# Kernel tuning notes

Hardware: AMD Instinct MI355X
Metric: run time of the kernel (lower is better)

## Reference

```python
import jax, jax.numpy as jnp
import numpy as np

B, N, C = 8, 4096, 768
H, M = 12, 64          # num_heads, num_landmarks
D = C // H             # head_dim = 64


def setup_inputs() -> dict:
    key = jax.random.key(0)
    k1, k2, k3, k4 = jax.random.split(key, 4)
    s = 0.02
    return {
        "x": jax.random.normal(k1, (B, N, C), dtype=jnp.float32),
        "w_qkv": jax.random.normal(k2, (3 * C, C), dtype=jnp.float32) * s,
        "w_proj": jax.random.normal(k3, (C, C), dtype=jnp.float32) * s,
        "b_proj": jax.random.normal(k4, (C,), dtype=jnp.float32) * s,
    }


def iterative_inv(mat, n_iter=6):
    # mat: [B, H, M, M]; Newton-Schulz cubic iteration for pseudo-inverse
    I = jnp.eye(mat.shape[-1], dtype=mat.dtype)
    K = mat
    # init: K^T / max_j(sum_i K_ij)  per (B,H)
    scale = jnp.max(jnp.sum(K, axis=-2), axis=-1)[:, :, None, None]
    V = jnp.swapaxes(K, -1, -2) / scale
    for _ in range(n_iter):
        KV = K @ V
        V = 0.25 * V @ (13.0 * I - KV @ (15.0 * I - KV @ (7.0 * I - KV)))
    return V


def reference(x, w_qkv, w_proj, b_proj):
    b, n, c = x.shape
    qkv = (x @ w_qkv.T).reshape(b, n, 3, H, D).transpose(2, 0, 3, 1, 4)  # [3,B,H,N,D]
    Q, K, V = qkv[0], qkv[1], qkv[2]
    Q = Q / (D ** 0.5)
    # landmark pooling (N % M == 0 path): segment means of length N//M
    Kl = K.reshape(b, H, M, n // M, D).mean(axis=-2)  # [B,H,M,D]
    Ql = Q.reshape(b, H, M, n // M, D).mean(axis=-2)  # [B,H,M,D]
    kernel1 = jax.nn.softmax(jnp.einsum('bhnd,bhmd->bhnm', Q, Kl), axis=-1)   # [B,H,N,M]
    kernel2 = jax.nn.softmax(jnp.einsum('bhmd,bhld->bhml', Ql, Kl), axis=-1)  # [B,H,M,M]
    kernel3 = jax.nn.softmax(jnp.einsum('bhmd,bhnd->bhmn', Ql, K), axis=-1)   # [B,H,M,N]
    SV = (kernel1 @ iterative_inv(kernel2)) @ (kernel3 @ V)  # [B,H,N,D]
    SV = SV.transpose(0, 2, 1, 3).reshape(b, n, c)
    out = SV @ w_proj.T + b_proj
    out = out + V.transpose(0, 2, 1, 3).reshape(b, n, c)
    return out
```

## Files before the change

kernel.cpp:

```cpp
#include <hip/hip_runtime.h>
#include <hip/hip_bf16.h>
#include <stdint.h>

typedef __bf16 bf16;
typedef __bf16 bf16x8 __attribute__((ext_vector_type(8)));
typedef __bf16 bf16x4 __attribute__((ext_vector_type(4)));
typedef float f32x4 __attribute__((ext_vector_type(4)));

#define B_ 8
#define N_ 4096
#define C_ 768
#define H_ 12
#define M_ 64
#define D_ 64
#define NT_ 32768
#define C3_ 2304

typedef __attribute__((address_space(3))) void lds_void_t;
typedef const __attribute__((address_space(1))) void gvoid_t;

__device__ __forceinline__ void gl_lds16(const void* gsrc, void* ldst) {
  __builtin_amdgcn_global_load_lds((gvoid_t*)(uintptr_t)gsrc,
                                   (lds_void_t*)(uintptr_t)ldst, 16, 0, 0);
}

__device__ __forceinline__ f32x4 mfma16(bf16x8 a, bf16x8 b, f32x4 c) {
  return __builtin_amdgcn_mfma_f32_16x16x32_bf16(a, b, c, 0, 0, 0);
}

__global__ void k_cvt(const float* __restrict__ in, bf16* __restrict__ out, int n4) {
  const int stride = gridDim.x * blockDim.x;
  for (int i = blockIdx.x * blockDim.x + threadIdx.x; i < n4; i += stride) {
    f32x4 v = *(const f32x4*)(in + (size_t)i * 4);
    bf16x4 o;
    o[0] = (bf16)v[0]; o[1] = (bf16)v[1]; o[2] = (bf16)v[2]; o[3] = (bf16)v[3];
    *(bf16x4*)(out + (size_t)i * 4) = o;
  }
}

__global__ __launch_bounds__(512, 2) void k_qkv(
    const bf16* __restrict__ xbf, const bf16* __restrict__ wbf,
    bf16* __restrict__ Qb, bf16* __restrict__ Kb, bf16* __restrict__ Vb,
    float* __restrict__ Qlf, float* __restrict__ Klf)
{
  __shared__ bf16 As[4][8192];
  __shared__ bf16 Bs[4][8192];
  const int t = threadIdx.x;
  const int wave = t >> 6, lane = t & 63;
  const int l15 = lane & 15, l16 = lane >> 4;

  const int bid = blockIdx.x;
  const int swz = (bid & 7) * 144 + (bid >> 3);
  const int bt = swz / 9;
  const int ct = swz % 9;
  const int row0 = bt * 256, col0 = ct * 256;
  const int wr = wave >> 2, wc = wave & 3;

  const int srow = t >> 2;
  const int scol = (((t & 3) ^ ((t >> 3) & 3)) << 3);
  const bf16* gaBase = xbf + (size_t)(row0 + srow) * C_ + scol;
  const bf16* gbBase = wbf + (size_t)(col0 + srow) * C_ + scol;

  const int arow = wr * 128 + l15;
  const int aoff = arow * 32 + ((l16 ^ ((l15 >> 1) & 3)) << 3);
  const int brow = wc * 64 + l15;
  const int boff = brow * 32 + ((l16 ^ ((l15 >> 1) & 3)) << 3);

  f32x4 acc[8][4] = {};

#define BAR() { __builtin_amdgcn_sched_barrier(0); __builtin_amdgcn_s_barrier(); __builtin_amdgcn_sched_barrier(0); }
#define VMW8 asm volatile("s_waitcnt vmcnt(8)" ::: "memory")
#define VMW4 asm volatile("s_waitcnt vmcnt(4)" ::: "memory")
#define VMW0 asm volatile("s_waitcnt vmcnt(0)" ::: "memory")

#define STAGE_HALF(kt3, c) {                                                     \
    const int sb_ = (kt3) & 3;                                                   \
    gl_lds16(gaBase + (size_t)((c) * 128) * C_ + (kt3) * 32,                     \
             &As[sb_][(c) * 4096 + t * 8]);                                      \
    gl_lds16(gbBase + (size_t)((c) * 128) * C_ + (kt3) * 32,                     \
             &Bs[sb_][(c) * 4096 + t * 8]); }

#define KSTEP(kt, DO_STAGE, VMW_) {                                              \
    const bf16* as_ = As[(kt) & 3];                                              \
    const bf16* bs_ = Bs[(kt) & 3];                                              \
    if (DO_STAGE) STAGE_HALF((kt) + 3, 0);                                       \
    bf16x8 bfr[4], afr[4];                                                       \
    _Pragma("unroll")                                                            \
    for (int j = 0; j < 4; ++j) bfr[j] = *(const bf16x8*)&bs_[boff + j * 512];   \
    _Pragma("unroll")                                                            \
    for (int i = 0; i < 4; ++i) afr[i] = *(const bf16x8*)&as_[aoff + i * 512];   \
    BAR();                                                                       \
    __builtin_amdgcn_s_setprio(1);                                               \
    _Pragma("unroll")                                                            \
    for (int i = 0; i < 4; ++i)                                                  \
      _Pragma("unroll")                                                          \
      for (int j = 0; j < 4; ++j)                                                \
        acc[i][j] = mfma16(afr[i], bfr[j], acc[i][j]);                           \
    __builtin_amdgcn_s_setprio(0);                                               \
    BAR();                                                                       \
    if (DO_STAGE) STAGE_HALF((kt) + 3, 1);                                       \
    _Pragma("unroll")                                                            \
    for (int i = 0; i < 4; ++i)                                                  \
      afr[i] = *(const bf16x8*)&as_[aoff + (4 + i) * 512];                       \
    BAR();                                                                       \
    __builtin_amdgcn_s_setprio(1);                                               \
    _Pragma("unroll")                                                            \
    for (int i = 0; i < 4; ++i)                                                  \
      _Pragma("unroll")                                                          \
      for (int j = 0; j < 4; ++j)                                                \
        acc[4 + i][j] = mfma16(afr[i], bfr[j], acc[4 + i][j]);                   \
    __builtin_amdgcn_s_setprio(0);                                               \
    VMW_;                                                                        \
    BAR(); }

  STAGE_HALF(0, 0); STAGE_HALF(0, 1);
  STAGE_HALF(1, 0); STAGE_HALF(1, 1);
  STAGE_HALF(2, 0); STAGE_HALF(2, 1);
  VMW8;
  BAR();

  for (int kt = 0; kt < 21; ++kt) { KSTEP(kt, true, VMW8); }
  KSTEP(21, false, VMW4);
  KSTEP(22, false, VMW0);
  KSTEP(23, false, (void)0);

#undef KSTEP
#undef STAGE_HALF

  const int colblock = col0 + wc * 64;
  const int which = colblock / C_;
  const int h = (colblock % C_) / D_;
  const int b = row0 >> 12;
  const int n_base = (row0 & (N_ - 1)) + wr * 128;
  bf16* dst = (which == 0) ? Qb : (which == 1) ? Kb : Vb;
  const float scale = (which == 0) ? 0.125f : 1.0f;
  const size_t base = ((size_t)(b * H_ + h) * N_ + n_base) * D_;
#pragma unroll
  for (int i = 0; i < 8; ++i)
#pragma unroll
    for (int q = 0; q < 4; ++q) {
      const int rloc = i * 16 + l16 * 4 + q;
#pragma unroll
      for (int j = 0; j < 4; ++j) {
        const int d = j * 16 + l15;
        dst[base + (size_t)rloc * D_ + d] = (bf16)(acc[i][j][q] * scale);
      }
    }
  if (which < 2) {
    float* lmout = (which == 0) ? Qlf : Klf;
#pragma unroll
    for (int g = 0; g < 2; ++g) {
      const int m = (n_base >> 6) + g;
#pragma unroll
      for (int j = 0; j < 4; ++j) {
        float s = 0.f;
#pragma unroll
        for (int i = 4 * g; i < 4 * g + 4; ++i)
#pragma unroll
          for (int q = 0; q < 4; ++q) s += acc[i][j][q];
        s *= scale;
        s += __shfl_xor(s, 16);
        s += __shfl_xor(s, 32);
        if (l16 == 0)
          lmout[((size_t)(b * H_ + h) * M_ + m) * D_ + j * 16 + lane] = s * (1.0f / 64.0f);
      }
    }
  }
}

__global__ __launch_bounds__(512, 1) void k_inv(
    const float* __restrict__ Qlf, const float* __restrict__ Klf,
    float* __restrict__ pinv)
{
  __shared__ float K2[4096];
  __shared__ float Vm[4096];
  __shared__ float KV[4096];
  __shared__ float T1[4096];
  __shared__ float U1[4096];
  __shared__ float tmp64[64];
  __shared__ float sscale;
  const int t = threadIdx.x;
  const int bh = blockIdx.x;
  const size_t off = (size_t)bh * 4096;
  for (int idx = t; idx < 4096; idx += 512) T1[idx] = Qlf[off + idx];
  for (int idx = t; idx < 4096; idx += 512) {
    const int r = idx >> 6, c = idx & 63;
    U1[c * 64 + r] = Klf[off + idx];
  }
  __syncthreads();
  const int j0 = (t & 15) * 4;
  const int i0 = (t >> 4) * 2;

  auto MMstep = [&](const float* A, const float* Bm, float* O, float dg, float sg, float al) {
    float r2[2][4] = {};
    for (int k = 0; k < 64; ++k) {
      f32x4 bv = *(const f32x4*)&Bm[k * 64 + j0];
      const float a0 = A[(i0 + 0) * 64 + k];
      const float a1 = A[(i0 + 1) * 64 + k];
#pragma unroll
      for (int jj = 0; jj < 4; ++jj) { r2[0][jj] += a0 * bv[jj]; r2[1][jj] += a1 * bv[jj]; }
    }
#pragma unroll
    for (int ii = 0; ii < 2; ++ii)
#pragma unroll
      for (int jj = 0; jj < 4; ++jj)
        O[(i0 + ii) * 64 + j0 + jj] = al * (dg * A[(i0 + ii) * 64 + (j0 + jj)] + sg * r2[ii][jj]);
    __syncthreads();
  };

  {
    float r2[2][4] = {};
    for (int k = 0; k < 64; ++k) {
      f32x4 bv = *(const f32x4*)&U1[k * 64 + j0];
      const float a0 = T1[(i0 + 0) * 64 + k];
      const float a1 = T1[(i0 + 1) * 64 + k];
#pragma unroll
      for (int jj = 0; jj < 4; ++jj) { r2[0][jj] += a0 * bv[jj]; r2[1][jj] += a1 * bv[jj]; }
    }
#pragma unroll
    for (int ii = 0; ii < 2; ++ii)
#pragma unroll
      for (int jj = 0; jj < 4; ++jj)
        K2[(i0 + ii) * 64 + j0 + jj] = __expf(r2[ii][jj]);
  }
  __syncthreads();
  if (t < 64) {
    float s = 0.f;
    for (int k = 0; k < 64; ++k) s += K2[t * 64 + k];
    tmp64[t] = 1.0f / s;
  }
  __syncthreads();
  for (int idx = t; idx < 4096; idx += 512) K2[idx] *= tmp64[idx >> 6];
  __syncthreads();
  if (t < 64) {
    float s = 0.f;
    for (int i = 0; i < 64; ++i) s += K2[i * 64 + t];
    tmp64[t] = s;
  }
  __syncthreads();
  if (t == 0) {
    float mx = tmp64[0];
    for (int j2 = 1; j2 < 64; ++j2) mx = fmaxf(mx, tmp64[j2]);
    sscale = 1.0f / mx;
  }
  __syncthreads();
  for (int idx = t; idx < 4096; idx += 512) {
    const int r = idx >> 6, c = idx & 63;
    Vm[idx] = K2[c * 64 + r] * sscale;
  }
  __syncthreads();

  float* pV = Vm;
  float* pT = T1;
  for (int it = 0; it < 6; ++it) {
    MMstep(K2, pV, KV, 0.f, 1.f, 1.f);
    MMstep(KV, KV, pT, 7.f, -1.f, 1.f);
    MMstep(KV, pT, U1, 15.f, -1.f, 1.f);
    MMstep(pV, U1, pT, 13.f, -1.f, 0.25f);
    float* sw = pV; pV = pT; pT = sw;
  }
  for (int idx = t; idx < 4096; idx += 512) pinv[off + idx] = pV[idx];
}

__global__ __launch_bounds__(256, 2) void k_k3v(
    const bf16* __restrict__ Qlb, const bf16* __restrict__ Kb, const bf16* __restrict__ Vb,
    float* __restrict__ Zacc, float* __restrict__ rowsum_g)
{
  __shared__ bf16 Qls[64 * 64];
  __shared__ bf16 Ks[128 * 64];
  __shared__ bf16 Vs[128 * 64];
  __shared__ bf16 Ps[64 * 128];
  __shared__ float rs[64];
  const int t = threadIdx.x, wave = t >> 6, lane = t & 63;
  const int bh = blockIdx.x >> 3;
  const int chunk = blockIdx.x & 7;
  const size_t kvbase = (size_t)bh * N_ * D_ + (size_t)chunk * 512 * D_;
  {
    const bf16* g = Qlb + (size_t)bh * 4096;
    gl_lds16(g + t * 8, &Qls[t * 8]);
    gl_lds16(g + (t + 256) * 8, &Qls[(t + 256) * 8]);
  }
  if (t < 64) rs[t] = 0.f;
  f32x4 z[4] = {};
  for (int st = 0; st < 4; ++st) {
    const bf16* gk = Kb + kvbase + (size_t)st * 128 * D_;
    const bf16* gv = Vb + kvbase + (size_t)st * 128 * D_;
#pragma unroll
    for (int c = 0; c < 4; ++c) {
      gl_lds16(gk + (t + c * 256) * 8, &Ks[(t + c * 256) * 8]);
      gl_lds16(gv + (t + c * 256) * 8, &Vs[(t + c * 256) * 8]);
    }
    __syncthreads();
    f32x4 sacc[4][2] = {};
#pragma unroll
    for (int kk = 0; kk < 2; ++kk) {
      bf16x8 af[4], bk[2];
#pragma unroll
      for (int i = 0; i < 4; ++i)
        af[i] = *(const bf16x8*)&Qls[(i * 16 + (lane & 15)) * 64 + kk * 32 + 8 * (lane >> 4)];
#pragma unroll
      for (int j2 = 0; j2 < 2; ++j2)
        bk[j2] = *(const bf16x8*)&Ks[(wave * 32 + j2 * 16 + (lane & 15)) * 64 + kk * 32 + 8 * (lane >> 4)];
#pragma unroll
      for (int i = 0; i < 4; ++i)
#pragma unroll
        for (int j2 = 0; j2 < 2; ++j2)
          sacc[i][j2] = mfma16(af[i], bk[j2], sacc[i][j2]);
    }
#pragma unroll
    for (int i = 0; i < 4; ++i)
#pragma unroll
      for (int q = 0; q < 4; ++q) {
        const float e0 = __expf(sacc[i][0][q]);
        const float e1 = __expf(sacc[i][1][q]);
        const int m = i * 16 + (lane >> 4) * 4 + q;
        Ps[m * 128 + wave * 32 + (lane & 15)] = (bf16)e0;
        Ps[m * 128 + wave * 32 + 16 + (lane & 15)] = (bf16)e1;
        float p = e0 + e1;
        p += __shfl_xor(p, 1); p += __shfl_xor(p, 2);
        p += __shfl_xor(p, 4); p += __shfl_xor(p, 8);
        if ((lane & 15) == 0) atomicAdd(&rs[m], p);
      }
    __syncthreads();
#pragma unroll
    for (int kk = 0; kk < 4; ++kk) {
      const int kbase = kk * 32 + 8 * (lane >> 4);
      const int d = wave * 16 + (lane & 15);
      bf16x8 bv;
#pragma unroll
      for (int e = 0; e < 8; ++e) bv[e] = Vs[(kbase + e) * 64 + d];
#pragma unroll
      for (int i = 0; i < 4; ++i) {
        bf16x8 ap = *(const bf16x8*)&Ps[(i * 16 + (lane & 15)) * 128 + kbase];
        z[i] = mfma16(ap, bv, z[i]);
      }
    }
    __syncthreads();
  }
  const size_t zbase = (size_t)bh * 4096;
#pragma unroll
  for (int i = 0; i < 4; ++i)
#pragma unroll
    for (int q = 0; q < 4; ++q) {
      const int m = i * 16 + (lane >> 4) * 4 + q;
      const int d = wave * 16 + (lane & 15);
      atomicAdd(&Zacc[zbase + m * 64 + d], z[i][q]);
    }
  if (t < 64) atomicAdd(&rowsum_g[bh * 64 + t], rs[t]);
}

__global__ __launch_bounds__(256, 1) void k_comb(
    const float* __restrict__ pinv, const float* __restrict__ Zacc,
    const float* __restrict__ rowsum_g, bf16* __restrict__ Wtb)
{
  __shared__ float Pv[4096];
  __shared__ float Zn[4096];
  const int t = threadIdx.x, bh = blockIdx.x;
  const size_t off = (size_t)bh * 4096;
  for (int idx = t; idx < 4096; idx += 256) Pv[idx] = pinv[off + idx];
  for (int idx = t; idx < 4096; idx += 256)
    Zn[idx] = Zacc[off + idx] / rowsum_g[bh * 64 + (idx >> 6)];
  __syncthreads();
  const int j0 = (t & 15) * 4, i0 = (t >> 4) * 4;
  float r[4][4] = {{0.f}};
  for (int k = 0; k < 64; ++k) {
    f32x4 bv = *(const f32x4*)&Zn[k * 64 + j0];
    float a[4];
#pragma unroll
    for (int ii = 0; ii < 4; ++ii) a[ii] = Pv[(i0 + ii) * 64 + k];
#pragma unroll
    for (int ii = 0; ii < 4; ++ii)
#pragma unroll
      for (int jj = 0; jj < 4; ++jj) r[ii][jj] += a[ii] * bv[jj];
  }
#pragma unroll
  for (int ii = 0; ii < 4; ++ii)
#pragma unroll
    for (int jj = 0; jj < 4; ++jj)
      Wtb[off + (size_t)(j0 + jj) * 64 + (i0 + ii)] = (bf16)r[ii][jj];
}

__global__ __launch_bounds__(256, 2) void k_sv(
    const bf16* __restrict__ Qb, const bf16* __restrict__ Klb,
    const bf16* __restrict__ Wtb, bf16* __restrict__ SVb)
{
  __shared__ bf16 Qs[128 * 64];
  __shared__ bf16 Kls[64 * 64];
  __shared__ bf16 Wts[64 * 64];
  __shared__ bf16 Ps[128 * 64];
  const int t = threadIdx.x, wave = t >> 6, lane = t & 63;
  const int bh = blockIdx.x >> 5;
  const int nt = blockIdx.x & 31;
  const int b = bh / H_, h = bh % H_;
  {
    const bf16* gq = Qb + (size_t)bh * N_ * D_ + (size_t)nt * 128 * D_;
#pragma unroll
    for (int c = 0; c < 4; ++c) gl_lds16(gq + (t + c * 256) * 8, &Qs[(t + c * 256) * 8]);
    const bf16* gkl = Klb + (size_t)bh * 4096;
    gl_lds16(gkl + t * 8, &Kls[t * 8]);
    gl_lds16(gkl + (t + 256) * 8, &Kls[(t + 256) * 8]);
    const bf16* gw = Wtb + (size_t)bh * 4096;
    gl_lds16(gw + t * 8, &Wts[t * 8]);
    gl_lds16(gw + (t + 256) * 8, &Wts[(t + 256) * 8]);
  }
  __syncthreads();
  f32x4 sacc[2][4] = {};
#pragma unroll
  for (int kk = 0; kk < 2; ++kk) {
    bf16x8 af[2], bl[4];
#pragma unroll
    for (int r = 0; r < 2; ++r)
      af[r] = *(const bf16x8*)&Qs[(wave * 32 + r * 16 + (lane & 15)) * 64 + kk * 32 + 8 * (lane >> 4)];
#pragma unroll
    for (int j = 0; j < 4; ++j)
      bl[j] = *(const bf16x8*)&Kls[(j * 16 + (lane & 15)) * 64 + kk * 32 + 8 * (lane >> 4)];
#pragma unroll
    for (int r = 0; r < 2; ++r)
#pragma unroll
      for (int j = 0; j < 4; ++j)
        sacc[r][j] = mfma16(af[r], bl[j], sacc[r][j]);
  }
#pragma unroll
  for (int r = 0; r < 2; ++r)
#pragma unroll
    for (int q = 0; q < 4; ++q) {
      float e[4]; float s = 0.f;
#pragma unroll
      for (int j = 0; j < 4; ++j) { e[j] = __expf(sacc[r][j][q]); s += e[j]; }
      s += __shfl_xor(s, 1); s += __shfl_xor(s, 2);
      s += __shfl_xor(s, 4); s += __shfl_xor(s, 8);
      const float is = 1.0f / s;
      const int row = wave * 32 + r * 16 + (lane >> 4) * 4 + q;
#pragma unroll
      for (int j = 0; j < 4; ++j)
        Ps[row * 64 + j * 16 + (lane & 15)] = (bf16)(e[j] * is);
    }
  __syncthreads();
  f32x4 oacc[2][4] = {};
#pragma unroll
  for (int kk = 0; kk < 2; ++kk) {
    bf16x8 af[2], bw[4];
#pragma unroll
    for (int r = 0; r < 2; ++r)
      af[r] = *(const bf16x8*)&Ps[(wave * 32 + r * 16 + (lane & 15)) * 64 + kk * 32 + 8 * (lane >> 4)];
#pragma unroll
    for (int j = 0; j < 4; ++j)
      bw[j] = *(const bf16x8*)&Wts[(j * 16 + (lane & 15)) * 64 + kk * 32 + 8 * (lane >> 4)];
#pragma unroll
    for (int r = 0; r < 2; ++r)
#pragma unroll
      for (int j = 0; j < 4; ++j)
        oacc[r][j] = mfma16(af[r], bw[j], oacc[r][j]);
  }
  const size_t outbase = ((size_t)b * N_ + (size_t)nt * 128) * C_ + h * 64;
#pragma unroll
  for (int r = 0; r < 2; ++r)
#pragma unroll
    for (int q = 0; q < 4; ++q) {
      const int row = wave * 32 + r * 16 + (lane >> 4) * 4 + q;
#pragma unroll
      for (int j = 0; j < 4; ++j)
        SVb[outbase + (size_t)row * C_ + j * 16 + (lane & 15)] = (bf16)(oacc[r][j][q]);
    }
}

__global__ __launch_bounds__(256, 2) void k_proj(
    const bf16* __restrict__ SVb, const bf16* __restrict__ wpb,
    const float* __restrict__ bproj, const bf16* __restrict__ Vb,
    float* __restrict__ outp)
{
  __shared__ bf16 As[2][128 * 32];
  __shared__ bf16 Bs[2][128 * 32];
  const int t = threadIdx.x;
  const int wave = t >> 6, lane = t & 63;
  const int bt = blockIdx.x & 255;
  const int ct = blockIdx.x >> 8;
  const int row0 = bt * 128, col0 = ct * 128;
  const int srow = t >> 2;
  const int scol = (t & 3) * 8;
  const bf16* ga = SVb + (size_t)row0 * C_ + scol;
  const bf16* gb = wpb + (size_t)col0 * C_ + scol;
  const int wr = wave >> 1, wc = wave & 1;

  f32x4 acc[4][4] = {};

#define PROJ_STAGE(bi, k0)                                                     \
  {                                                                            \
    gl_lds16(ga + (size_t)srow * C_ + (k0), &As[bi][t * 8]);                   \
    gl_lds16(ga + (size_t)(srow + 64) * C_ + (k0), &As[bi][(t + 256) * 8]);    \
    gl_lds16(gb + (size_t)srow * C_ + (k0), &Bs[bi][t * 8]);                   \
    gl_lds16(gb + (size_t)(srow + 64) * C_ + (k0), &Bs[bi][(t + 256) * 8]);    \
  }

  PROJ_STAGE(0, 0);
  __syncthreads();
  for (int ks = 0; ks < 24; ++ks) {
    const int buf = ks & 1;
    if (ks < 23) PROJ_STAGE(buf ^ 1, (ks + 1) * 32);
    bf16x8 af[4], bfr[4];
#pragma unroll
    for (int i = 0; i < 4; ++i) {
      af[i]  = *(const bf16x8*)&As[buf][(wr * 64 + i * 16 + (lane & 15)) * 32 + 8 * (lane >> 4)];
      bfr[i] = *(const bf16x8*)&Bs[buf][(wc * 64 + i * 16 + (lane & 15)) * 32 + 8 * (lane >> 4)];
    }
#pragma unroll
    for (int i = 0; i < 4; ++i)
#pragma unroll
      for (int j = 0; j < 4; ++j)
        acc[i][j] = mfma16(af[i], bfr[j], acc[i][j]);
    __syncthreads();
  }
#undef PROJ_STAGE

#pragma unroll
  for (int i = 0; i < 4; ++i)
#pragma unroll
    for (int q = 0; q < 4; ++q) {
      const int row = row0 + wr * 64 + i * 16 + (lane >> 4) * 4 + q;
      const int b = row >> 12, n = row & (N_ - 1);
#pragma unroll
      for (int j = 0; j < 4; ++j) {
        const int col = col0 + wc * 64 + j * 16 + (lane & 15);
        const int h = col >> 6, d = col & 63;
        const float v = acc[i][j][q] + bproj[col] +
                        (float)Vb[((size_t)(b * H_ + h) * N_ + n) * D_ + d];
        outp[(size_t)row * C_ + col] = v;
      }
    }
}

extern "C" void kernel_launch(void* const* d_in, const int* in_sizes, int n_in,
                              void* d_out, int out_size, void* d_ws, size_t ws_size,
                              hipStream_t stream) {
  const float* x = (const float*)d_in[0];
  const float* wqkv = (const float*)d_in[1];
  const float* wproj = (const float*)d_in[2];
  const float* bproj = (const float*)d_in[3];
  float* outp = (float*)d_out;
  char* ws = (char*)d_ws;

  size_t off = 0;
  auto take = [&](size_t bytes) { char* p = ws + off; off += bytes; return p; };
  bf16* xbf     = (bf16*)take(50331648);
  bf16* wqkvbf  = (bf16*)take(3538944);
  bf16* wprojbf = (bf16*)take(1179648);
  bf16* Qb      = (bf16*)take(50331648);
  bf16* Kb      = (bf16*)take(50331648);
  bf16* Vb      = (bf16*)take(50331648);
  float* Qlf    = (float*)take(1572864);
  float* Klf    = (float*)take(1572864);
  bf16* Qlb     = (bf16*)take(786432);
  bf16* Klb     = (bf16*)take(786432);
  float* pinvp  = (float*)take(1572864);
  float* Zacc   = (float*)take(1572864);
  float* rowsum = (float*)take(24576);
  bf16* Wtb     = (bf16*)take(786432);
  bf16* SVb     = xbf;

  hipMemsetAsync(Zacc, 0, 1572864 + 24576, stream);

  k_cvt<<<2048, 256, 0, stream>>>(x, xbf, 25165824 / 4);
  k_cvt<<<432, 256, 0, stream>>>(wqkv, wqkvbf, 1769472 / 4);
  k_cvt<<<144, 256, 0, stream>>>(wproj, wprojbf, 589824 / 4);
  k_qkv<<<1152, 512, 0, stream>>>(xbf, wqkvbf, Qb, Kb, Vb, Qlf, Klf);
  k_cvt<<<96, 256, 0, stream>>>(Qlf, Qlb, 393216 / 4);
  k_cvt<<<96, 256, 0, stream>>>(Klf, Klb, 393216 / 4);
  k_inv<<<96, 512, 0, stream>>>(Qlf, Klf, pinvp);
  k_k3v<<<768, 256, 0, stream>>>(Qlb, Kb, Vb, Zacc, rowsum);
  k_comb<<<96, 256, 0, stream>>>(pinvp, Zacc, rowsum, Wtb);
  k_sv<<<96 * 32, 256, 0, stream>>>(Qb, Klb, Wtb, SVb);
  k_proj<<<256 * 6, 256, 0, stream>>>(SVb, wprojbf, bproj, Vb, outp);
}
```

Measured before the change: 409.6 us.

## Single-barrier 4-stage GEMM pipelines, swizzled proj, fold landmark bf16 casts

```diff
diff --git a/kernel.cpp b/kernel.cpp
--- a/kernel.cpp
+++ b/kernel.cpp
@@ -27,6 +27,12 @@
 __device__ __forceinline__ f32x4 mfma16(bf16x8 a, bf16x8 b, f32x4 c) {
   return __builtin_amdgcn_mfma_f32_16x16x32_bf16(a, b, c, 0, 0, 0);
 }
+
+#define VMW8 asm volatile("s_waitcnt vmcnt(8)" ::: "memory")
+#define VMW4 asm volatile("s_waitcnt vmcnt(4)" ::: "memory")
+#define VMW0 asm volatile("s_waitcnt vmcnt(0)" ::: "memory")
+#define LGKM0 asm volatile("s_waitcnt lgkmcnt(0)" ::: "memory")
+#define RAWBAR() { __builtin_amdgcn_s_barrier(); __builtin_amdgcn_sched_barrier(0); }
 
 __global__ void k_cvt(const float* __restrict__ in, bf16* __restrict__ out, int n4) {
   const int stride = gridDim.x * blockDim.x;
@@ -51,8 +57,7 @@
 
   const int bid = blockIdx.x;
   const int swz = (bid & 7) * 144 + (bid >> 3);
-  const int bt = swz / 9;
-  const int ct = swz % 9;
+  const int bt = swz / 9, ct = swz % 9;
   const int row0 = bt * 256, col0 = ct * 256;
   const int wr = wave >> 2, wc = wave & 3;
 
@@ -61,71 +66,63 @@
   const bf16* gaBase = xbf + (size_t)(row0 + srow) * C_ + scol;
   const bf16* gbBase = wbf + (size_t)(col0 + srow) * C_ + scol;
 
-  const int arow = wr * 128 + l15;
-  const int aoff = arow * 32 + ((l16 ^ ((l15 >> 1) & 3)) << 3);
-  const int brow = wc * 64 + l15;
-  const int boff = brow * 32 + ((l16 ^ ((l15 >> 1) & 3)) << 3);
+  const int aoff = (wr * 128 + l15) * 32 + ((l16 ^ ((l15 >> 1) & 3)) << 3);
+  const int boff = (wc * 64 + l15) * 32 + ((l16 ^ ((l15 >> 1) & 3)) << 3);
 
   f32x4 acc[8][4] = {};
 
-#define BAR() { __builtin_amdgcn_sched_barrier(0); __builtin_amdgcn_s_barrier(); __builtin_amdgcn_sched_barrier(0); }
-#define VMW8 asm volatile("s_waitcnt vmcnt(8)" ::: "memory")
-#define VMW4 asm volatile("s_waitcnt vmcnt(4)" ::: "memory")
-#define VMW0 asm volatile("s_waitcnt vmcnt(0)" ::: "memory")
-
-#define STAGE_HALF(kt3, c) {                                                     \
+#define QSTAGE(kt3) {                                                            \
     const int sb_ = (kt3) & 3;                                                   \
-    gl_lds16(gaBase + (size_t)((c) * 128) * C_ + (kt3) * 32,                     \
-             &As[sb_][(c) * 4096 + t * 8]);                                      \
-    gl_lds16(gbBase + (size_t)((c) * 128) * C_ + (kt3) * 32,                     \
-             &Bs[sb_][(c) * 4096 + t * 8]); }
-
-#define KSTEP(kt, DO_STAGE, VMW_) {                                              \
+    gl_lds16(gaBase + (size_t)0 * C_ + (kt3) * 32, &As[sb_][t * 8]);             \
+    gl_lds16(gbBase + (size_t)0 * C_ + (kt3) * 32, &Bs[sb_][t * 8]);             \
+    gl_lds16(gaBase + (size_t)128 * C_ + (kt3) * 32, &As[sb_][(t + 512) * 8]);   \
+    gl_lds16(gbBase + (size_t)128 * C_ + (kt3) * 32, &Bs[sb_][(t + 512) * 8]); }
+
+#define QKSTEP(kt, DO_STAGE, VMW_) {                                             \
     const bf16* as_ = As[(kt) & 3];                                              \
     const bf16* bs_ = Bs[(kt) & 3];                                              \
-    if (DO_STAGE) STAGE_HALF((kt) + 3, 0);                                       \
-    bf16x8 bfr[4], afr[4];                                                       \
+    if (DO_STAGE) QSTAGE((kt) + 3);                                              \
+    bf16x8 bfr[4], afr[8];                                                       \
     _Pragma("unroll")                                                            \
     for (int j = 0; j < 4; ++j) bfr[j] = *(const bf16x8*)&bs_[boff + j * 512];   \
     _Pragma("unroll")                                                            \
-    for (int i = 0; i < 4; ++i) afr[i] = *(const bf16x8*)&as_[aoff + i * 512];   \
-    BAR();                                                                       \
+    for (int i = 0; i < 8; ++i) afr[i] = *(const bf16x8*)&as_[aoff + i * 512];   \
     __builtin_amdgcn_s_setprio(1);                                               \
     _Pragma("unroll")                                                            \
-    for (int i = 0; i < 4; ++i)                                                  \
+    for (int i = 0; i < 8; ++i)                                                  \
       _Pragma("unroll")                                                          \
       for (int j = 0; j < 4; ++j)                                                \
         acc[i][j] = mfma16(afr[i], bfr[j], acc[i][j]);                           \
     __builtin_amdgcn_s_setprio(0);                                               \
-    BAR();                                                                       \
-    if (DO_STAGE) STAGE_HALF((kt) + 3, 1);                                       \
-    _Pragma("unroll")                                                            \
-    for (int i = 0; i < 4; ++i)                                                  \
-      afr[i] = *(const bf16x8*)&as_[aoff + (4 + i) * 512];                       \
-    BAR();                                                                       \
-    __builtin_amdgcn_s_setprio(1);                                               \
-    _Pragma("unroll")                                                            \
-    for (int i = 0; i < 4; ++i)                                                  \
-      _Pragma("unroll")                                                          \
-      for (int j = 0; j < 4; ++j)                                                \
-        acc[4 + i][j] = mfma16(afr[i], bfr[j], acc[4 + i][j]);                   \
-    __builtin_amdgcn_s_setprio(0);                                               \
     VMW_;                                                                        \
-    BAR(); }
-
-  STAGE_HALF(0, 0); STAGE_HALF(0, 1);
-  STAGE_HALF(1, 0); STAGE_HALF(1, 1);
-  STAGE_HALF(2, 0); STAGE_HALF(2, 1);
+    LGKM0;                                                                       \
+    RAWBAR(); }
+
+  QSTAGE(0); QSTAGE(1); QSTAGE(2);
   VMW8;
-  BAR();
-
-  for (int kt = 0; kt < 21; ++kt) { KSTEP(kt, true, VMW8); }
-  KSTEP(21, false, VMW4);
-  KSTEP(22, false, VMW0);
-  KSTEP(23, false, (void)0);
-
-#undef KSTEP
-#undef STAGE_HALF
+  RAWBAR();
+
+#pragma unroll 4
+  for (int kt = 0; kt < 20; ++kt) { QKSTEP(kt, true, VMW8); }
+  QKSTEP(20, true, VMW8);
+  QKSTEP(21, false, VMW4);
+  QKSTEP(22, false, VMW0);
+  {
+    const bf16* as_ = As[23 & 3];
+    const bf16* bs_ = Bs[23 & 3];
+    bf16x8 bfr[4], afr[8];
+#pragma unroll
+    for (int j = 0; j < 4; ++j) bfr[j] = *(const bf16x8*)&bs_[boff + j * 512];
+#pragma unroll
+    for (int i = 0; i < 8; ++i) afr[i] = *(const bf16x8*)&as_[aoff + i * 512];
+#pragma unroll
+    for (int i = 0; i < 8; ++i)
+#pragma unroll
+      for (int j = 0; j < 4; ++j)
+        acc[i][j] = mfma16(afr[i], bfr[j], acc[i][j]);
+  }
+#undef QKSTEP
+#undef QSTAGE
 
   const int colblock = col0 + wc * 64;
   const int which = colblock / C_;
@@ -170,7 +167,7 @@
 
 __global__ __launch_bounds__(512, 1) void k_inv(
     const float* __restrict__ Qlf, const float* __restrict__ Klf,
-    float* __restrict__ pinv)
+    float* __restrict__ pinv, bf16* __restrict__ Qlb, bf16* __restrict__ Klb)
 {
   __shared__ float K2[4096];
   __shared__ float Vm[4096];
@@ -182,10 +179,16 @@
   const int t = threadIdx.x;
   const int bh = blockIdx.x;
   const size_t off = (size_t)bh * 4096;
-  for (int idx = t; idx < 4096; idx += 512) T1[idx] = Qlf[off + idx];
+  for (int idx = t; idx < 4096; idx += 512) {
+    const float q = Qlf[off + idx];
+    T1[idx] = q;
+    Qlb[off + idx] = (bf16)q;
+  }
   for (int idx = t; idx < 4096; idx += 512) {
     const int r = idx >> 6, c = idx & 63;
-    U1[c * 64 + r] = Klf[off + idx];
+    const float k = Klf[off + idx];
+    U1[c * 64 + r] = k;
+    Klb[off + idx] = (bf16)k;
   }
   __syncthreads();
   const int j0 = (t & 15) * 4;
@@ -469,58 +472,89 @@
     const float* __restrict__ bproj, const bf16* __restrict__ Vb,
     float* __restrict__ outp)
 {
-  __shared__ bf16 As[2][128 * 32];
-  __shared__ bf16 Bs[2][128 * 32];
+  __shared__ bf16 As[4][4096];
+  __shared__ bf16 Bs[4][4096];
   const int t = threadIdx.x;
   const int wave = t >> 6, lane = t & 63;
-  const int bt = blockIdx.x & 255;
-  const int ct = blockIdx.x >> 8;
+  const int l15 = lane & 15, l16 = lane >> 4;
+  const int bid = blockIdx.x;
+  const int swz = (bid & 7) * 192 + (bid >> 3);
+  const int bt = swz / 6, ct = swz % 6;
   const int row0 = bt * 128, col0 = ct * 128;
+  const int wr = wave >> 1, wc = wave & 1;
+
   const int srow = t >> 2;
-  const int scol = (t & 3) * 8;
-  const bf16* ga = SVb + (size_t)row0 * C_ + scol;
-  const bf16* gb = wpb + (size_t)col0 * C_ + scol;
-  const int wr = wave >> 1, wc = wave & 1;
+  const int scol = (((t & 3) ^ ((t >> 3) & 3)) << 3);
+  const bf16* ga = SVb + (size_t)(row0 + srow) * C_ + scol;
+  const bf16* gb = wpb + (size_t)(col0 + srow) * C_ + scol;
+
+  const int aoff = (wr * 64 + l15) * 32 + ((l16 ^ ((l15 >> 1) & 3)) << 3);
+  const int boff = (wc * 64 + l15) * 32 + ((l16 ^ ((l15 >> 1) & 3)) << 3);
 
   f32x4 acc[4][4] = {};
 
-#define PROJ_STAGE(bi, k0)                                                     \
-  {                                                                            \
-    gl_lds16(ga + (size_t)srow * C_ + (k0), &As[bi][t * 8]);                   \
-    gl_lds16(ga + (size_t)(srow + 64) * C_ + (k0), &As[bi][(t + 256) * 8]);    \
-    gl_lds16(gb + (size_t)srow * C_ + (k0), &Bs[bi][t * 8]);                   \
-    gl_lds16(gb + (size_t)(srow + 64) * C_ + (k0), &Bs[bi][(t + 256) * 8]);    \
-  }
-
-  PROJ_STAGE(0, 0);
-  __syncthreads();
-  for (int ks = 0; ks < 24; ++ks) {
-    const int buf = ks & 1;
-    if (ks < 23) PROJ_STAGE(buf ^ 1, (ks + 1) * 32);
-    bf16x8 af[4], bfr[4];
-#pragma unroll
-    for (int i = 0; i < 4; ++i) {
-      af[i]  = *(const bf16x8*)&As[buf][(wr * 64 + i * 16 + (lane & 15)) * 32 + 8 * (lane >> 4)];
-      bfr[i] = *(const bf16x8*)&Bs[buf][(wc * 64 + i * 16 + (lane & 15)) * 32 + 8 * (lane >> 4)];
-    }
+#define PSTAGE(kt3) {                                                          \
+    const int sb_ = (kt3) & 3;                                                 \
+    gl_lds16(ga + (size_t)0 * C_ + (kt3) * 32, &As[sb_][t * 8]);               \
+    gl_lds16(gb + (size_t)0 * C_ + (kt3) * 32, &Bs[sb_][t * 8]);               \
+    gl_lds16(ga + (size_t)64 * C_ + (kt3) * 32, &As[sb_][(t + 256) * 8]);      \
+    gl_lds16(gb + (size_t)64 * C_ + (kt3) * 32, &Bs[sb_][(t + 256) * 8]); }
+
+#define PKSTEP(kt, DO_STAGE, VMW_) {                                           \
+    const bf16* as_ = As[(kt) & 3];                                            \
+    const bf16* bs_ = Bs[(kt) & 3];                                            \
+    if (DO_STAGE) PSTAGE((kt) + 3);                                            \
+    bf16x8 afr[4], bfr[4];                                                     \
+    _Pragma("unroll")                                                          \
+    for (int j = 0; j < 4; ++j) bfr[j] = *(const bf16x8*)&bs_[boff + j * 512]; \
+    _Pragma("unroll")                                                          \
+    for (int i = 0; i < 4; ++i) afr[i] = *(const bf16x8*)&as_[aoff + i * 512]; \
+    __builtin_amdgcn_s_setprio(1);                                             \
+    _Pragma("unroll")                                                          \
+    for (int i = 0; i < 4; ++i)                                                \
+      _Pragma("unroll")                                                        \
+      for (int j = 0; j < 4; ++j)                                              \
+        acc[i][j] = mfma16(afr[i], bfr[j], acc[i][j]);                         \
+    __builtin_amdgcn_s_setprio(0);                                             \
+    VMW_;                                                                      \
+    LGKM0;                                                                     \
+    RAWBAR(); }
+
+  PSTAGE(0); PSTAGE(1); PSTAGE(2);
+  VMW8;
+  RAWBAR();
+
+#pragma unroll 4
+  for (int kt = 0; kt < 20; ++kt) { PKSTEP(kt, true, VMW8); }
+  PKSTEP(20, true, VMW8);
+  PKSTEP(21, false, VMW4);
+  PKSTEP(22, false, VMW0);
+  {
+    const bf16* as_ = As[3];
+    const bf16* bs_ = Bs[3];
+    bf16x8 afr[4], bfr[4];
+#pragma unroll
+    for (int j = 0; j < 4; ++j) bfr[j] = *(const bf16x8*)&bs_[boff + j * 512];
+#pragma unroll
+    for (int i = 0; i < 4; ++i) afr[i] = *(const bf16x8*)&as_[aoff + i * 512];
 #pragma unroll
     for (int i = 0; i < 4; ++i)
 #pragma unroll
       for (int j = 0; j < 4; ++j)
-        acc[i][j] = mfma16(af[i], bfr[j], acc[i][j]);
-    __syncthreads();
-  }
-#undef PROJ_STAGE
+        acc[i][j] = mfma16(afr[i], bfr[j], acc[i][j]);
+  }
+#undef PKSTEP
+#undef PSTAGE
 
 #pragma unroll
   for (int i = 0; i < 4; ++i)
 #pragma unroll
     for (int q = 0; q < 4; ++q) {
-      const int row = row0 + wr * 64 + i * 16 + (lane >> 4) * 4 + q;
+      const int row = row0 + wr * 64 + i * 16 + l16 * 4 + q;
       const int b = row >> 12, n = row & (N_ - 1);
 #pragma unroll
       for (int j = 0; j < 4; ++j) {
-        const int col = col0 + wc * 64 + j * 16 + (lane & 15);
+        const int col = col0 + wc * 64 + j * 16 + l15;
         const int h = col >> 6, d = col & 63;
         const float v = acc[i][j][q] + bproj[col] +
                         (float)Vb[((size_t)(b * H_ + h) * N_ + n) * D_ + d];
@@ -563,11 +597,9 @@
   k_cvt<<<432, 256, 0, stream>>>(wqkv, wqkvbf, 1769472 / 4);
   k_cvt<<<144, 256, 0, stream>>>(wproj, wprojbf, 589824 / 4);
   k_qkv<<<1152, 512, 0, stream>>>(xbf, wqkvbf, Qb, Kb, Vb, Qlf, Klf);
-  k_cvt<<<96, 256, 0, stream>>>(Qlf, Qlb, 393216 / 4);
-  k_cvt<<<96, 256, 0, stream>>>(Klf, Klb, 393216 / 4);
-  k_inv<<<96, 512, 0, stream>>>(Qlf, Klf, pinvp);
+  k_inv<<<96, 512, 0, stream>>>(Qlf, Klf, pinvp, Qlb, Klb);
   k_k3v<<<768, 256, 0, stream>>>(Qlb, Kb, Vb, Zacc, rowsum);
   k_comb<<<96, 256, 0, stream>>>(pinvp, Zacc, rowsum, Wtb);
   k_sv<<<96 * 32, 256, 0, stream>>>(Qb, Klb, Wtb, SVb);
-  k_proj<<<256 * 6, 256, 0, stream>>>(SVb, wprojbf, bproj, Vb, outp);
-}
+  k_proj<<<1536, 256, 0, stream>>>(SVb, wprojbf, bproj, Vb, outp);
+}
```

Measured after the change: 392.0 us. 1.04x faster.
